# Optimization experiments

Hardware: AMD Instinct MI355X
Metric: run time of the kernel (lower is better)

Reference implementation:

```python
import jax, jax.numpy as jnp
import numpy as np

N_HEADS = 16


def _rope_tables(seq_len, head_dim, dtype):
    # matches torch RoPE.__init__: inv_freq over head_dim, outer with positions
    inv_freq = 1.0 / (10000.0 ** (jnp.arange(0, head_dim, 2, dtype=jnp.float32) / head_dim))
    t = jnp.arange(seq_len, dtype=jnp.float32)
    freqs = jnp.outer(t, inv_freq)  # [T, head_dim//2]
    return jnp.cos(freqs).astype(dtype), jnp.sin(freqs).astype(dtype)


def _apply_rope(x, cos, sin):
    # x: [B, H, T, Dh]; interleaved even/odd rotation
    x_even = x[..., ::2]
    x_odd = x[..., 1::2]
    rot_even = x_even * cos - x_odd * sin
    rot_odd = x_even * sin + x_odd * cos
    return jnp.stack([rot_even, rot_odd], axis=-1).reshape(x.shape)


def setup_inputs() -> dict:
    key = jax.random.key(0)
    ks = jax.random.split(key, 5)
    B, T, D = 4, 1024, 1024
    s = 1.0 / np.sqrt(D)
    return {
        "x": jax.random.normal(ks[0], (B, T, D), dtype=jnp.float32),
        "Wq": jax.random.normal(ks[1], (D, D), dtype=jnp.float32) * s,
        "Wk": jax.random.normal(ks[2], (D, D), dtype=jnp.float32) * s,
        "Wv": jax.random.normal(ks[3], (D, D), dtype=jnp.float32) * s,
        "Wo": jax.random.normal(ks[4], (D, D), dtype=jnp.float32) * s,
    }


def reference(x, Wq, Wk, Wv, Wo):
    B, T, D = x.shape
    H = N_HEADS
    Dh = D // H

    def proj(W):
        # nn.Linear: x @ W.T ; reshape to [B, H, T, Dh]
        return (x @ W.T).reshape(B, T, H, Dh).transpose(0, 2, 1, 3)

    q, k, v = proj(Wq), proj(Wk), proj(Wv)
    cos, sin = _rope_tables(T, Dh, x.dtype)
    q = _apply_rope(q, cos, sin)
    k = _apply_rope(k, cos, sin)

    # NOTE: original module applies NO 1/sqrt(Dh) scaling
    scores = jnp.einsum("bhqd,bhkd->bhqk", q, k)
    causal = jnp.tril(jnp.ones((T, T), dtype=bool))
    scores = jnp.where(causal, scores, -jnp.inf)
    attn = jax.nn.softmax(scores, axis=-1)
    out = jnp.einsum("bhqk,bhkd->bhqd", attn, v)
    out = out.transpose(0, 2, 1, 3).reshape(B, T, D)
    return out @ Wo.T
```

## Files before the change

### kernel.cpp

```cpp
#include <hip/hip_runtime.h>
#include <stdint.h>

typedef unsigned short u16;
typedef short s16x8 __attribute__((ext_vector_type(8)));
typedef __bf16 bf16x8 __attribute__((ext_vector_type(8)));
typedef _Float16 f16x8 __attribute__((ext_vector_type(8)));
typedef float f32x4 __attribute__((ext_vector_type(4)));

#define SEQ    1024
#define DMODEL 1024
#define NB     4
#define NH     16
#define DH     64
#define QBLK   128
#define KVB    64
#define LOG2E  1.4426950408889634f

__device__ __forceinline__ u16 f2bf(float f) {
  uint32_t u = __builtin_bit_cast(uint32_t, f);
  u += 0x7fffu + ((u >> 16) & 1u);
  return (u16)(u >> 16);
}
__device__ __forceinline__ u16 f2bf_rz(float f) {
  return (u16)(__builtin_bit_cast(uint32_t, f) >> 16);
}
__device__ __forceinline__ float bf2f(u16 h) {
  uint32_t u = ((uint32_t)h) << 16;
  return __builtin_bit_cast(float, u);
}
__device__ __forceinline__ u16 f2h(float f) {
  return __builtin_bit_cast(u16, (_Float16)f);
}
__device__ __forceinline__ float h2f(u16 u) {
  return (float)__builtin_bit_cast(_Float16, u);
}

#define MFMA16(a, b, c)  __builtin_amdgcn_mfma_f32_16x16x32_bf16((a), (b), (c), 0, 0, 0)
#define MFMA16H(a, b, c) __builtin_amdgcn_mfma_f32_16x16x32_f16((a), (b), (c), 0, 0, 0)

template<bool F16>
__device__ __forceinline__ f32x4 MF(s16x8 a, s16x8 b, f32x4 c) {
  if constexpr (F16)
    return MFMA16H(__builtin_bit_cast(f16x8, a), __builtin_bit_cast(f16x8, b), c);
  else
    return MFMA16(__builtin_bit_cast(bf16x8, a), __builtin_bit_cast(bf16x8, b), c);
}

__device__ __forceinline__ void gload_lds16(const u16* g, uintptr_t lds_addr) {
  __builtin_amdgcn_global_load_lds(
      (__attribute__((address_space(1))) void*)(uintptr_t)g,
      (__attribute__((address_space(3))) void*)lds_addr,
      16, 0, 0);
}

__global__ void cast_all_kernel(
    const float* __restrict__ x, const float* __restrict__ wq,
    const float* __restrict__ wk, const float* __restrict__ wv,
    const float* __restrict__ wo,
    u16* __restrict__ xd, u16* __restrict__ wqd, u16* __restrict__ wkd,
    u16* __restrict__ wvd, u16* __restrict__ wod)
{
  const int NX = (NB * SEQ * DMODEL) / 8;
  const int NW = (DMODEL * DMODEL) / 8;
  int c = blockIdx.x * blockDim.x + threadIdx.x;
  const float* src; u16* dst; bool tobf = false;
  if (c < NX)                { src = x;  dst = xd; }
  else if ((c -= NX) < NW)   { src = wq; dst = wqd; }
  else if ((c -= NW) < NW)   { src = wk; dst = wkd; }
  else if ((c -= NW) < NW)   { src = wv; dst = wvd; }
  else if ((c -= NW) < NW)   { src = wo; dst = wod; tobf = true; }
  else return;
  float f[8];
  float4 v0 = *(const float4*)(src + (size_t)c * 8);
  float4 v1 = *(const float4*)(src + (size_t)c * 8 + 4);
  f[0] = v0.x; f[1] = v0.y; f[2] = v0.z; f[3] = v0.w;
  f[4] = v1.x; f[5] = v1.y; f[6] = v1.z; f[7] = v1.w;
  union { u16 u[8]; uint4 v; } H;
#pragma unroll
  for (int e = 0; e < 8; ++e) H.u[e] = tobf ? f2bf(f[e]) : f2h(f[e]);
  *(uint4*)(dst + (size_t)c * 8) = H.v;
}

__global__ void rope_kernel(u16* __restrict__ Q, u16* __restrict__ K) {
  const int nP = (NB * SEQ) * (DMODEL / 2);
  int idx = blockIdx.x * blockDim.x + threadIdx.x;
  u16* buf; int p;
  if (idx < nP) { buf = Q; p = idx; }
  else          { buf = K; p = idx - nP; }
  int row = p >> 9;
  int pi  = p & 511;
  int t   = row & (SEQ - 1);
  int fi  = pi & 31;
  float inv = exp2f((float)fi * (-13.287712379549449f / 32.0f));
  float ang = (float)t * inv;
  float sn, cs;
  sincosf(ang, &sn, &cs);
  size_t off = (size_t)row * DMODEL + pi * 2;
  uint32_t v = *(uint32_t*)(buf + off);
  float e = h2f((u16)(v & 0xffffu));
  float o = h2f((u16)(v >> 16));
  float re = e * cs - o * sn;
  float ro = e * sn + o * cs;
  *(uint32_t*)(buf + off) = (uint32_t)f2h(re) | ((uint32_t)f2h(ro) << 16);
}

struct GemmPtrs {
  const u16* B[3]; u16* C0[3]; int mode[3];
};

template<bool F16, int BN>
__global__ __launch_bounds__(256) void gemm_bt_kernel(
    const u16* __restrict__ A,
    GemmPtrs P, float* __restrict__ CF,
    int M, int N, int K, int out_f32)
{
  constexpr int NF = BN / 32;
  constexpr int BCH = BN / 32;
  __shared__ __align__(16) u16 sA[2][128 * 64];
  __shared__ __align__(16) u16 sB[2][BN * 64];
  const int t = threadIdx.x, lane = t & 63;
  const int wave = t >> 6;
  const int g = lane >> 4, cl = lane & 15;
  const int z = blockIdx.z;
  const u16* B = P.B[z];
  const int n0 = blockIdx.x * BN, m0 = blockIdx.y * 128;
  const int wr = wave >> 1, wc = wave & 1;

  int srow[4], scol[4], soff[4];
#pragma unroll
  for (int j = 0; j < 4; ++j) {
    int c = j * 256 + t;
    srow[j] = c >> 3;
    scol[j] = ((c & 7) ^ (srow[j] & 7)) * 8;
    soff[j] = c * 16;
  }

  f32x4 acc[4][NF] = {};

#pragma unroll
  for (int j = 0; j < 4; ++j)
    gload_lds16(A + (size_t)(m0 + srow[j]) * K + scol[j], (uintptr_t)&sA[0][0] + soff[j]);
#pragma unroll
  for (int j = 0; j < BCH; ++j)
    gload_lds16(B + (size_t)(n0 + srow[j]) * K + scol[j], (uintptr_t)&sB[0][0] + soff[j]);

  int cur = 0;
  for (int k0 = 0; k0 < K; k0 += 64) {
    const bool hasnext = (k0 + 64 < K);
    if (hasnext) {
      const int nk = k0 + 64;
#pragma unroll
      for (int j = 0; j < 4; ++j)
        gload_lds16(A + (size_t)(m0 + srow[j]) * K + nk + scol[j],
                    (uintptr_t)&sA[cur ^ 1][0] + soff[j]);
#pragma unroll
      for (int j = 0; j < BCH; ++j)
        gload_lds16(B + (size_t)(n0 + srow[j]) * K + nk + scol[j],
                    (uintptr_t)&sB[cur ^ 1][0] + soff[j]);
      if constexpr (BN == 128) asm volatile("s_waitcnt vmcnt(8)" ::: "memory");
      else                     asm volatile("s_waitcnt vmcnt(6)" ::: "memory");
    } else {
      asm volatile("s_waitcnt vmcnt(0)" ::: "memory");
    }
    __builtin_amdgcn_s_barrier();

    s16x8 af[4][2];
#pragma unroll
    for (int m = 0; m < 4; ++m) {
      int row = wr * 64 + m * 16 + cl;
#pragma unroll
      for (int kk = 0; kk < 2; ++kk)
        af[m][kk] = *(const s16x8*)&sA[cur][row * 64 + (((kk * 4 + g) ^ (row & 7)) * 8)];
    }
#pragma unroll
    for (int n = 0; n < NF; ++n) {
      int row = wc * (BN / 2) + n * 16 + cl;
      s16x8 b0 = *(const s16x8*)&sB[cur][row * 64 + ((g ^ (row & 7)) * 8)];
      s16x8 b1 = *(const s16x8*)&sB[cur][row * 64 + (((4 + g) ^ (row & 7)) * 8)];
#pragma unroll
      for (int m = 0; m < 4; ++m) {
        acc[m][n] = MF<F16>(af[m][0], b0, acc[m][n]);
        acc[m][n] = MF<F16>(af[m][1], b1, acc[m][n]);
      }
    }
    __builtin_amdgcn_s_barrier();
    cur ^= 1;
  }

  if (out_f32) {
#pragma unroll
    for (int m = 0; m < 4; ++m)
#pragma unroll
      for (int n = 0; n < NF; ++n)
#pragma unroll
        for (int r = 0; r < 4; ++r) {
          int row = m0 + wr * 64 + m * 16 + g * 4 + r;
          int col = n0 + wc * (BN / 2) + n * 16 + cl;
          CF[(size_t)row * N + col] = acc[m][n][r];
        }
  } else if (P.mode[z] == 1) {
    u16* VT = P.C0[z];
#pragma unroll
    for (int m = 0; m < 4; ++m)
#pragma unroll
      for (int n = 0; n < NF; ++n) {
        int row0 = m0 + wr * 64 + m * 16 + g * 4;
        int col = n0 + wc * (BN / 2) + n * 16 + cl;
        union { u16 u[4]; uint2 v; } pk;
#pragma unroll
        for (int r = 0; r < 4; ++r) pk.u[r] = f2bf(acc[m][n][r]);
        *(uint2*)&VT[(size_t)col * M + row0] = pk.v;
      }
  } else {
    u16* C = P.C0[z];
#pragma unroll
    for (int m = 0; m < 4; ++m)
#pragma unroll
      for (int n = 0; n < NF; ++n)
#pragma unroll
        for (int r = 0; r < 4; ++r) {
          int row = m0 + wr * 64 + m * 16 + g * 4 + r;
          int col = n0 + wc * (BN / 2) + n * 16 + cl;
          float v = acc[m][n][r];
          C[(size_t)row * N + col] = F16 ? f2h(v) : f2bf(v);
        }
  }
}

__global__ __launch_bounds__(256, 2) void attn_kernel(
    const u16* __restrict__ Q, const u16* __restrict__ K,
    const u16* __restrict__ Vt,
    u16* __restrict__ Oh)
{
  __shared__ __align__(16) u16 sK [2][KVB * 64];
  __shared__ __align__(16) u16 sVt[2][DH * KVB];
  __shared__ __align__(16) u16 sP[128 * 72];

  const int t = threadIdx.x, lane = t & 63, wave = t >> 6;
  const int g = lane >> 4, cl = lane & 15;
  const int h = blockIdx.x & (NH - 1), b = blockIdx.x >> 4;
  const int y = blockIdx.y;
  const int qi = (y < 4) ? (7 - y) : (y - 4);
  const int q0 = qi * QBLK;
  const size_t rowbase = (size_t)b * SEQ;
  const int colbase = h * DH;
  const int MT = NB * SEQ;

  const u16* Kb  = K + rowbase * DMODEL + colbase;
  const u16* Vtb = Vt + (size_t)(h * DH) * MT + b * SEQ;

  int srow[2], scol[2], soff[2];
#pragma unroll
  for (int j = 0; j < 2; ++j) {
    int c = j * 256 + t;
    srow[j] = c >> 3;
    scol[j] = ((c & 7) ^ (srow[j] & 7)) * 8;
    soff[j] = c * 16;
  }

  int koff0[4], koff1[4];
#pragma unroll
  for (int n = 0; n < 4; ++n) {
    int row = n * 16 + cl;
    koff0[n] = row * 64 + ((g ^ (row & 7)) * 8);
    koff1[n] = row * 64 + (((4 + g) ^ (row & 7)) * 8);
  }
  int paoff[2][2];
#pragma unroll
  for (int kk = 0; kk < 2; ++kk) {
    paoff[kk][0] = (wave * 32 + cl) * 72 + kk * 32 + g * 8;
    paoff[kk][1] = (wave * 32 + 16 + cl) * 72 + kk * 32 + g * 8;
  }

  f16x8 qf[2][2];
#pragma unroll
  for (int mf = 0; mf < 2; ++mf) {
    int qrow = q0 + wave * 32 + mf * 16 + cl;
    const u16* pq = Q + (rowbase + qrow) * DMODEL + colbase + g * 8;
    qf[mf][0] = __builtin_bit_cast(f16x8, *(const s16x8*)pq);
    qf[mf][1] = __builtin_bit_cast(f16x8, *(const s16x8*)(pq + 32));
  }

  bf16x8 ones;
#pragma unroll
  for (int e = 0; e < 8; ++e) ones[e] = (__bf16)1.0f;

  f32x4 o_acc[2][4] = {};
  f32x4 o_l[2] = {};

  const int last = 2 * qi + 1;
  const int wrow0 = q0 + wave * 32;
  const int prow0 = wave * 32;

#pragma unroll
  for (int j = 0; j < 2; ++j) {
    gload_lds16(Kb + (size_t)srow[j] * DMODEL + scol[j],  (uintptr_t)&sK[0][0] + soff[j]);
    gload_lds16(Vtb + (size_t)srow[j] * MT + scol[j],     (uintptr_t)&sVt[0][0] + soff[j]);
  }
  __syncthreads();

  int cur = 0;
  for (int kt = 0; kt <= last; ++kt) {
    const int kv0 = kt * KVB;
    if (kt < last) {
      const int nk = kv0 + KVB;
#pragma unroll
      for (int j = 0; j < 2; ++j) {
        gload_lds16(Kb + (size_t)(nk + srow[j]) * DMODEL + scol[j],
                    (uintptr_t)&sK[cur ^ 1][0] + soff[j]);
        gload_lds16(Vtb + (size_t)srow[j] * MT + nk + scol[j],
                    (uintptr_t)&sVt[cur ^ 1][0] + soff[j]);
      }
    }

    const bool skip = (wrow0 + 31) < kv0;
    if (!skip) {
      const bool needmask = (kv0 + 63) > wrow0;

      f32x4 s[2][4];
      __builtin_amdgcn_s_setprio(1);
#pragma unroll
      for (int n = 0; n < 4; ++n) {
        f16x8 k0 = __builtin_bit_cast(f16x8, *(const s16x8*)&sK[cur][koff0[n]]);
        f16x8 k1 = __builtin_bit_cast(f16x8, *(const s16x8*)&sK[cur][koff1[n]]);
#pragma unroll
        for (int mf = 0; mf < 2; ++mf) {
          f32x4 zz = {};
          zz = MFMA16H(qf[mf][0], k0, zz);
          zz = MFMA16H(qf[mf][1], k1, zz);
          s[mf][n] = zz;
        }
      }
      __builtin_amdgcn_s_setprio(0);

#pragma unroll
      for (int mf = 0; mf < 2; ++mf) {
#pragma unroll
        for (int r = 0; r < 4; ++r) {
          int qg = wrow0 + mf * 16 + g * 4 + r;
          int prow = prow0 + mf * 16 + g * 4 + r;
#pragma unroll
          for (int n = 0; n < 4; ++n) {
            float p = exp2f(s[mf][n][r] * LOG2E);
            if (needmask && (kv0 + n * 16 + cl > qg)) p = 0.0f;
            sP[prow * 72 + n * 16 + cl] = f2bf_rz(p);
          }
        }
      }

      __builtin_amdgcn_s_setprio(1);
#pragma unroll
      for (int kk = 0; kk < 2; ++kk) {
        bf16x8 pa0 = *(const bf16x8*)&sP[paoff[kk][0]];
        bf16x8 pa1 = *(const bf16x8*)&sP[paoff[kk][1]];
#pragma unroll
        for (int n = 0; n < 4; ++n) {
          bf16x8 vf = *(const bf16x8*)&sVt[cur][(kk == 0) ? koff0[n] : koff1[n]];
          o_acc[0][n] = MFMA16(pa0, vf, o_acc[0][n]);
          o_acc[1][n] = MFMA16(pa1, vf, o_acc[1][n]);
        }
        o_l[0] = MFMA16(pa0, ones, o_l[0]);
        o_l[1] = MFMA16(pa1, ones, o_l[1]);
      }
      __builtin_amdgcn_s_setprio(0);
    }

    __syncthreads();
    cur ^= 1;
  }

#pragma unroll
  for (int mf = 0; mf < 2; ++mf)
#pragma unroll
    for (int n = 0; n < 4; ++n)
#pragma unroll
      for (int r = 0; r < 4; ++r) {
        float ov = o_acc[mf][n][r] / o_l[mf][r];
        int qrow = q0 + wave * 32 + mf * 16 + g * 4 + r;
        size_t idx = (rowbase + qrow) * DMODEL + colbase + n * 16 + cl;
        Oh[idx] = f2bf(ov);
      }
}

extern "C" void kernel_launch(void* const* d_in, const int* in_sizes, int n_in,
                              void* d_out, int out_size, void* d_ws, size_t ws_size,
                              hipStream_t stream) {
  const float* x  = (const float*)d_in[0];
  const float* Wq = (const float*)d_in[1];
  const float* Wk = (const float*)d_in[2];
  const float* Wv = (const float*)d_in[3];
  const float* Wo = (const float*)d_in[4];
  float* out = (float*)d_out;

  const int M = NB * SEQ;
  const int D = DMODEL;
  char* ws = (char*)d_ws;
  const size_t MB = 1u << 20;
  u16* xh16 = (u16*)(ws + 0 * MB);
  u16* qh16 = (u16*)(ws + 8 * MB);
  u16* kh16 = (u16*)(ws + 16 * MB);
  u16* vt   = (u16*)(ws + 24 * MB);
  u16* oh   = (u16*)(ws + 40 * MB);
  u16* wq16 = (u16*)(ws + 48 * MB);
  u16* wk16 = (u16*)(ws + 50 * MB);
  u16* wv16 = (u16*)(ws + 52 * MB);
  u16* wob  = (u16*)(ws + 54 * MB);

  {
    int total = M * D / 8 + 4 * (D * D / 8);
    cast_all_kernel<<<(total + 255) / 256, 256, 0, stream>>>(
        x, Wq, Wk, Wv, Wo, xh16, wq16, wk16, wv16, wob);
  }

  {
    GemmPtrs P;
    P.B[0] = wq16; P.B[1] = wk16; P.B[2] = wv16;
    P.C0[0] = qh16; P.C0[1] = kh16; P.C0[2] = vt;
    P.mode[0] = 0; P.mode[1] = 0; P.mode[2] = 1;
    gemm_bt_kernel<true, 128><<<dim3(D / 128, M / 128, 3), 256, 0, stream>>>(
        xh16, P, nullptr, M, D, D, 0);
  }

  rope_kernel<<<(2 * M * (D / 2) + 255) / 256, 256, 0, stream>>>(qh16, kh16);

  attn_kernel<<<dim3(NH * NB, 8), 256, 0, stream>>>(qh16, kh16, vt, oh);

  {
    GemmPtrs P;
    P.B[0] = wob; P.B[1] = wob; P.B[2] = wob;
    P.C0[0] = nullptr; P.C0[1] = nullptr; P.C0[2] = nullptr;
    P.mode[0] = 0; P.mode[1] = 0; P.mode[2] = 0;
    gemm_bt_kernel<false, 64><<<dim3(D / 64, M / 128, 1), 256, 0, stream>>>(
        oh, P, out, M, D, D, 1);
  }
}
```

Baseline: 103.4 us.

## Fuse Q RoPE into attention and pair Q/K projections sharing A tiles

Q rotary embedding now happens inside the attention kernel's Q fragment load, so the separate RoPE pass touches only K. The QKV projection becomes a kernel where one block computes both the Q and K tiles from a single shared A tile, and a second z-slice computes V. In exchange, the new kernel drops the double-buffered cp.async-style pipeline for a single buffer with two syncthreads per step. The V blocks do half the work of the Q/K blocks, which unbalances the grid.

```diff
diff --git a/kernel.cpp b/kernel.cpp
--- a/kernel.cpp
+++ b/kernel.cpp
@@ -15,6 +15,7 @@
 #define QBLK   128
 #define KVB    64
 #define LOG2E  1.4426950408889634f
+#define ROPE_C (-13.287712379549449f / 32.0f)
 
 __device__ __forceinline__ u16 f2bf(float f) {
   uint32_t u = __builtin_bit_cast(uint32_t, f);
@@ -81,48 +82,140 @@
   *(uint4*)(dst + (size_t)c * 8) = H.v;
 }
 
-__global__ void rope_kernel(u16* __restrict__ Q, u16* __restrict__ K) {
-  const int nP = (NB * SEQ) * (DMODEL / 2);
-  int idx = blockIdx.x * blockDim.x + threadIdx.x;
-  u16* buf; int p;
-  if (idx < nP) { buf = Q; p = idx; }
-  else          { buf = K; p = idx - nP; }
+__global__ void rope_k_kernel(u16* __restrict__ K) {
+  int p = blockIdx.x * blockDim.x + threadIdx.x;
   int row = p >> 9;
   int pi  = p & 511;
   int t   = row & (SEQ - 1);
   int fi  = pi & 31;
-  float inv = exp2f((float)fi * (-13.287712379549449f / 32.0f));
+  float inv = exp2f((float)fi * ROPE_C);
   float ang = (float)t * inv;
   float sn, cs;
   sincosf(ang, &sn, &cs);
   size_t off = (size_t)row * DMODEL + pi * 2;
-  uint32_t v = *(uint32_t*)(buf + off);
+  uint32_t v = *(uint32_t*)(K + off);
   float e = h2f((u16)(v & 0xffffu));
   float o = h2f((u16)(v >> 16));
   float re = e * cs - o * sn;
   float ro = e * sn + o * cs;
-  *(uint32_t*)(buf + off) = (uint32_t)f2h(re) | ((uint32_t)f2h(ro) << 16);
-}
-
-struct GemmPtrs {
-  const u16* B[3]; u16* C0[3]; int mode[3];
-};
-
-template<bool F16, int BN>
-__global__ __launch_bounds__(256) void gemm_bt_kernel(
-    const u16* __restrict__ A,
-    GemmPtrs P, float* __restrict__ CF,
-    int M, int N, int K, int out_f32)
+  *(uint32_t*)(K + off) = (uint32_t)f2h(re) | ((uint32_t)f2h(ro) << 16);
+}
+
+__global__ __launch_bounds__(256, 2) void qkv_kernel(
+    const u16* __restrict__ A, const u16* __restrict__ Bq,
+    const u16* __restrict__ Bk, const u16* __restrict__ Bv,
+    u16* __restrict__ Cq, u16* __restrict__ Ck, u16* __restrict__ VT,
+    int M, int N, int K)
 {
-  constexpr int NF = BN / 32;
-  constexpr int BCH = BN / 32;
+  __shared__ __align__(16) u16 sA [128 * 64];
+  __shared__ __align__(16) u16 sB0[128 * 64];
+  __shared__ __align__(16) u16 sB1[128 * 64];
+  const int t = threadIdx.x, lane = t & 63;
+  const int wave = t >> 6;
+  const int g = lane >> 4, cl = lane & 15;
+  const bool pair = (blockIdx.z == 0);
+  const int n0 = blockIdx.x * 128, m0 = blockIdx.y * 128;
+  const int wr = wave >> 1, wc = wave & 1;
+
+  int srow[4], scol[4], soff[4];
+#pragma unroll
+  for (int j = 0; j < 4; ++j) {
+    int c = j * 256 + t;
+    srow[j] = c >> 3;
+    scol[j] = ((c & 7) ^ (srow[j] & 7)) * 8;
+    soff[j] = c * 16;
+  }
+
+  f32x4 acc0[4][4] = {};
+  f32x4 acc1[4][4] = {};
+
+  for (int k0 = 0; k0 < K; k0 += 64) {
+#pragma unroll
+    for (int j = 0; j < 4; ++j)
+      gload_lds16(A + (size_t)(m0 + srow[j]) * K + k0 + scol[j], (uintptr_t)sA + soff[j]);
+    if (pair) {
+#pragma unroll
+      for (int j = 0; j < 4; ++j) {
+        gload_lds16(Bq + (size_t)(n0 + srow[j]) * K + k0 + scol[j], (uintptr_t)sB0 + soff[j]);
+        gload_lds16(Bk + (size_t)(n0 + srow[j]) * K + k0 + scol[j], (uintptr_t)sB1 + soff[j]);
+      }
+    } else {
+#pragma unroll
+      for (int j = 0; j < 4; ++j)
+        gload_lds16(Bv + (size_t)(n0 + srow[j]) * K + k0 + scol[j], (uintptr_t)sB0 + soff[j]);
+    }
+    __syncthreads();
+
+    s16x8 af[4][2];
+#pragma unroll
+    for (int m = 0; m < 4; ++m) {
+      int row = wr * 64 + m * 16 + cl;
+#pragma unroll
+      for (int kk = 0; kk < 2; ++kk)
+        af[m][kk] = *(const s16x8*)&sA[row * 64 + (((kk * 4 + g) ^ (row & 7)) * 8)];
+    }
+#pragma unroll
+    for (int n = 0; n < 4; ++n) {
+      int row = wc * 64 + n * 16 + cl;
+      int o0 = row * 64 + ((g ^ (row & 7)) * 8);
+      int o1 = row * 64 + (((4 + g) ^ (row & 7)) * 8);
+      s16x8 b0 = *(const s16x8*)&sB0[o0];
+      s16x8 b1 = *(const s16x8*)&sB0[o1];
+#pragma unroll
+      for (int m = 0; m < 4; ++m) {
+        acc0[m][n] = MF<true>(af[m][0], b0, acc0[m][n]);
+        acc0[m][n] = MF<true>(af[m][1], b1, acc0[m][n]);
+      }
+      if (pair) {
+        s16x8 c0 = *(const s16x8*)&sB1[o0];
+        s16x8 c1 = *(const s16x8*)&sB1[o1];
+#pragma unroll
+        for (int m = 0; m < 4; ++m) {
+          acc1[m][n] = MF<true>(af[m][0], c0, acc1[m][n]);
+          acc1[m][n] = MF<true>(af[m][1], c1, acc1[m][n]);
+        }
+      }
+    }
+    __syncthreads();
+  }
+
+  if (pair) {
+#pragma unroll
+    for (int m = 0; m < 4; ++m)
+#pragma unroll
+      for (int n = 0; n < 4; ++n)
+#pragma unroll
+        for (int r = 0; r < 4; ++r) {
+          int row = m0 + wr * 64 + m * 16 + g * 4 + r;
+          int col = n0 + wc * 64 + n * 16 + cl;
+          Cq[(size_t)row * N + col] = f2h(acc0[m][n][r]);
+          Ck[(size_t)row * N + col] = f2h(acc1[m][n][r]);
+        }
+  } else {
+#pragma unroll
+    for (int m = 0; m < 4; ++m)
+#pragma unroll
+      for (int n = 0; n < 4; ++n) {
+        int row0 = m0 + wr * 64 + m * 16 + g * 4;
+        int col = n0 + wc * 64 + n * 16 + cl;
+        union { u16 u[4]; uint2 v; } pk;
+#pragma unroll
+        for (int r = 0; r < 4; ++r) pk.u[r] = f2bf(acc0[m][n][r]);
+        *(uint2*)&VT[(size_t)col * M + row0] = pk.v;
+      }
+  }
+}
+
+__global__ __launch_bounds__(256) void gemm_wo_kernel(
+    const u16* __restrict__ A, const u16* __restrict__ B,
+    float* __restrict__ CF, int M, int N, int K)
+{
+  constexpr int BN = 64;
   __shared__ __align__(16) u16 sA[2][128 * 64];
   __shared__ __align__(16) u16 sB[2][BN * 64];
   const int t = threadIdx.x, lane = t & 63;
   const int wave = t >> 6;
   const int g = lane >> 4, cl = lane & 15;
-  const int z = blockIdx.z;
-  const u16* B = P.B[z];
   const int n0 = blockIdx.x * BN, m0 = blockIdx.y * 128;
   const int wr = wave >> 1, wc = wave & 1;
 
@@ -135,13 +228,13 @@
     soff[j] = c * 16;
   }
 
-  f32x4 acc[4][NF] = {};
+  f32x4 acc[4][2] = {};
 
 #pragma unroll
   for (int j = 0; j < 4; ++j)
     gload_lds16(A + (size_t)(m0 + srow[j]) * K + scol[j], (uintptr_t)&sA[0][0] + soff[j]);
 #pragma unroll
-  for (int j = 0; j < BCH; ++j)
+  for (int j = 0; j < 2; ++j)
     gload_lds16(B + (size_t)(n0 + srow[j]) * K + scol[j], (uintptr_t)&sB[0][0] + soff[j]);
 
   int cur = 0;
@@ -154,11 +247,10 @@
         gload_lds16(A + (size_t)(m0 + srow[j]) * K + nk + scol[j],
                     (uintptr_t)&sA[cur ^ 1][0] + soff[j]);
 #pragma unroll
-      for (int j = 0; j < BCH; ++j)
+      for (int j = 0; j < 2; ++j)
         gload_lds16(B + (size_t)(n0 + srow[j]) * K + nk + scol[j],
                     (uintptr_t)&sB[cur ^ 1][0] + soff[j]);
-      if constexpr (BN == 128) asm volatile("s_waitcnt vmcnt(8)" ::: "memory");
-      else                     asm volatile("s_waitcnt vmcnt(6)" ::: "memory");
+      asm volatile("s_waitcnt vmcnt(6)" ::: "memory");
     } else {
       asm volatile("s_waitcnt vmcnt(0)" ::: "memory");
     }
@@ -173,58 +265,30 @@
         af[m][kk] = *(const s16x8*)&sA[cur][row * 64 + (((kk * 4 + g) ^ (row & 7)) * 8)];
     }
 #pragma unroll
-    for (int n = 0; n < NF; ++n) {
-      int row = wc * (BN / 2) + n * 16 + cl;
+    for (int n = 0; n < 2; ++n) {
+      int row = wc * 32 + n * 16 + cl;
       s16x8 b0 = *(const s16x8*)&sB[cur][row * 64 + ((g ^ (row & 7)) * 8)];
       s16x8 b1 = *(const s16x8*)&sB[cur][row * 64 + (((4 + g) ^ (row & 7)) * 8)];
 #pragma unroll
       for (int m = 0; m < 4; ++m) {
-        acc[m][n] = MF<F16>(af[m][0], b0, acc[m][n]);
-        acc[m][n] = MF<F16>(af[m][1], b1, acc[m][n]);
+        acc[m][n] = MF<false>(af[m][0], b0, acc[m][n]);
+        acc[m][n] = MF<false>(af[m][1], b1, acc[m][n]);
       }
     }
     __builtin_amdgcn_s_barrier();
     cur ^= 1;
   }
 
-  if (out_f32) {
-#pragma unroll
-    for (int m = 0; m < 4; ++m)
-#pragma unroll
-      for (int n = 0; n < NF; ++n)
-#pragma unroll
-        for (int r = 0; r < 4; ++r) {
-          int row = m0 + wr * 64 + m * 16 + g * 4 + r;
-          int col = n0 + wc * (BN / 2) + n * 16 + cl;
-          CF[(size_t)row * N + col] = acc[m][n][r];
-        }
-  } else if (P.mode[z] == 1) {
-    u16* VT = P.C0[z];
-#pragma unroll
-    for (int m = 0; m < 4; ++m)
-#pragma unroll
-      for (int n = 0; n < NF; ++n) {
-        int row0 = m0 + wr * 64 + m * 16 + g * 4;
-        int col = n0 + wc * (BN / 2) + n * 16 + cl;
-        union { u16 u[4]; uint2 v; } pk;
-#pragma unroll
-        for (int r = 0; r < 4; ++r) pk.u[r] = f2bf(acc[m][n][r]);
-        *(uint2*)&VT[(size_t)col * M + row0] = pk.v;
-      }
-  } else {
-    u16* C = P.C0[z];
-#pragma unroll
-    for (int m = 0; m < 4; ++m)
-#pragma unroll
-      for (int n = 0; n < NF; ++n)
-#pragma unroll
-        for (int r = 0; r < 4; ++r) {
-          int row = m0 + wr * 64 + m * 16 + g * 4 + r;
-          int col = n0 + wc * (BN / 2) + n * 16 + cl;
-          float v = acc[m][n][r];
-          C[(size_t)row * N + col] = F16 ? f2h(v) : f2bf(v);
-        }
-  }
+#pragma unroll
+  for (int m = 0; m < 4; ++m)
+#pragma unroll
+    for (int n = 0; n < 2; ++n)
+#pragma unroll
+      for (int r = 0; r < 4; ++r) {
+        int row = m0 + wr * 64 + m * 16 + g * 4 + r;
+        int col = n0 + wc * 32 + n * 16 + cl;
+        CF[(size_t)row * N + col] = acc[m][n][r];
+      }
 }
 
 __global__ __launch_bounds__(256, 2) void attn_kernel(
@@ -277,8 +341,22 @@
   for (int mf = 0; mf < 2; ++mf) {
     int qrow = q0 + wave * 32 + mf * 16 + cl;
     const u16* pq = Q + (rowbase + qrow) * DMODEL + colbase + g * 8;
-    qf[mf][0] = __builtin_bit_cast(f16x8, *(const s16x8*)pq);
-    qf[mf][1] = __builtin_bit_cast(f16x8, *(const s16x8*)(pq + 32));
+    s16x8 raw0 = *(const s16x8*)pq;
+    s16x8 raw1 = *(const s16x8*)(pq + 32);
+    f16x8 r0, r1;
+#pragma unroll
+    for (int j = 0; j < 4; ++j) {
+      float sn, cs;
+      sincosf((float)qrow * exp2f((float)(4 * g + j) * ROPE_C), &sn, &cs);
+      float e = h2f((u16)raw0[2 * j]), o = h2f((u16)raw0[2 * j + 1]);
+      r0[2 * j]     = (_Float16)(e * cs - o * sn);
+      r0[2 * j + 1] = (_Float16)(e * sn + o * cs);
+      sincosf((float)qrow * exp2f((float)(16 + 4 * g + j) * ROPE_C), &sn, &cs);
+      e = h2f((u16)raw1[2 * j]); o = h2f((u16)raw1[2 * j + 1]);
+      r1[2 * j]     = (_Float16)(e * cs - o * sn);
+      r1[2 * j + 1] = (_Float16)(e * sn + o * cs);
+    }
+    qf[mf][0] = r0; qf[mf][1] = r1;
   }
 
   bf16x8 ones;
@@ -412,25 +490,13 @@
         x, Wq, Wk, Wv, Wo, xh16, wq16, wk16, wv16, wob);
   }
 
-  {
-    GemmPtrs P;
-    P.B[0] = wq16; P.B[1] = wk16; P.B[2] = wv16;
-    P.C0[0] = qh16; P.C0[1] = kh16; P.C0[2] = vt;
-    P.mode[0] = 0; P.mode[1] = 0; P.mode[2] = 1;
-    gemm_bt_kernel<true, 128><<<dim3(D / 128, M / 128, 3), 256, 0, stream>>>(
-        xh16, P, nullptr, M, D, D, 0);
-  }
-
-  rope_kernel<<<(2 * M * (D / 2) + 255) / 256, 256, 0, stream>>>(qh16, kh16);
+  qkv_kernel<<<dim3(D / 128, M / 128, 2), 256, 0, stream>>>(
+      xh16, wq16, wk16, wv16, qh16, kh16, vt, M, D, D);
+
+  rope_k_kernel<<<(M * (D / 2)) / 256, 256, 0, stream>>>(kh16);
 
   attn_kernel<<<dim3(NH * NB, 8), 256, 0, stream>>>(qh16, kh16, vt, oh);
 
-  {
-    GemmPtrs P;
-    P.B[0] = wob; P.B[1] = wob; P.B[2] = wob;
-    P.C0[0] = nullptr; P.C0[1] = nullptr; P.C0[2] = nullptr;
-    P.mode[0] = 0; P.mode[1] = 0; P.mode[2] = 0;
-    gemm_bt_kernel<false, 64><<<dim3(D / 64, M / 128, 1), 256, 0, stream>>>(
-        oh, P, out, M, D, D, 1);
-  }
-}
+  gemm_wo_kernel<<<dim3(D / 64, M / 128, 1), 256, 0, stream>>>(
+      oh, wob, out, M, D, D);
+}
```

Measured after the change: 99.67 us, median of 2. -3.6%, faster.
